# Kernel optimization log

Hardware: AMD Instinct MI355X
Metric: run time of the kernel (lower is better)

The kernel has to match this reference:

```python
import jax, jax.numpy as jnp
import numpy as np

N_PIXELS = 262144
N_CENTERS = 1024
N_G = 256

def setup_inputs() -> dict:
    key = jax.random.key(0)
    k1, k2, k3, k4, k5 = jax.random.split(key, 5)
    return {
        "alphas": jax.random.normal(k1, (N_CENTERS, 1), dtype=jnp.float32),
        "betas": jax.random.normal(k2, (N_G, 2), dtype=jnp.float32) * 0.1,
        "K": jax.random.normal(k3, (N_PIXELS, N_G), dtype=jnp.float32) * 0.05,
        "all_pixels": jax.random.normal(k4, (N_PIXELS, 2), dtype=jnp.float32),
        "all_p_centers": jax.random.normal(k5, (N_CENTERS, 2), dtype=jnp.float32),
        "sdp2": jnp.ones((), dtype=jnp.float32) * 2.0,
    }

def reference(alphas, betas, K, all_pixels, all_p_centers, sdp2):
    # deformed pixel coordinates: (n_pixels, 2)
    deformed = all_pixels - K @ betas
    # pairwise squared distances via norm expansion (same math as the torch
    # ones-matmul broadcasting, expressed with plain broadcasting):
    p_norm2 = jnp.sum(jnp.square(deformed), axis=1, keepdims=True)      # (n_pixels, 1)
    c_norm2 = jnp.sum(jnp.square(all_p_centers), axis=1)                # (n_centers,)
    p_dot_c = 2.0 * (deformed @ all_p_centers.T)                        # (n_pixels, n_centers)
    big_matrix = p_norm2 + c_norm2[None, :] - p_dot_c
    kBp = jnp.exp(-big_matrix / (2.0 * sdp2))
    return kBp @ alphas                                                  # (n_pixels, 1)
```

## Files before the change

kernel.cpp:

```cpp
#include <hip/hip_runtime.h>

#if defined(__has_builtin)
#  if __has_builtin(__builtin_amdgcn_exp2f)
#    define EXP2F(x) __builtin_amdgcn_exp2f(x)
#  else
#    define EXP2F(x) exp2f(x)
#  endif
#else
#  define EXP2F(x) exp2f(x)
#endif

constexpr int NPIX  = 262144;
constexpr int NC    = 1024;
constexpr int NG    = 256;
constexpr int BLOCK = 256;
constexpr int PIX_PER_BLOCK = 256;

template <int CTRL>
__device__ __forceinline__ float dpp_add(float v) {
    union { float f; int i; } u, t;
    u.f = v;
    t.i = __builtin_amdgcn_update_dpp(0, u.i, CTRL, 0xF, 0xF, true);
    return v + t.f;
}
template <int CTRL>
__device__ __forceinline__ float dpp_mov(float v) {
    union { float f; int i; } u, t;
    u.f = v;
    t.i = __builtin_amdgcn_update_dpp(0, u.i, CTRL, 0xF, 0xF, true);
    return t.f;
}
__device__ __forceinline__ float sum16(float v) {
    v = dpp_add<0xB1>(v);
    v = dpp_add<0x4E>(v);
    v = dpp_add<0x141>(v);
    v = dpp_add<0x140>(v);
    return v;
}

__global__ void prep_centers(const float* __restrict__ alphas,
                             const float* __restrict__ centers,
                             const float* __restrict__ sdp2p,
                             float* __restrict__ ws)
{
    const int c = blockIdx.x * blockDim.x + threadIdx.x;
    if (c < NC) {
        const float f  = -1.44269504088896340736f / (2.0f * sdp2p[0]);
        const float cx = centers[2 * c + 0];
        const float cy = centers[2 * c + 1];
        ws[c]          = cx;
        ws[NC + c]     = cy;
        ws[2 * NC + c] = alphas[c] * EXP2F(f * (cx * cx + cy * cy));
    }
}

__global__ __launch_bounds__(BLOCK, 4)
void kbpa_main(const float* __restrict__ betas,
               const float* __restrict__ K,
               const float* __restrict__ pixels,
               const float* __restrict__ sdp2p,
               const float* __restrict__ ws,
               float* __restrict__ out)
{
    const int tid  = threadIdx.x;
    const int lane = tid & 63;
    const int wave = tid >> 6;
    const int l4   = lane & 15;
    const int lg   = lane >> 4;
    const int own  = l4 * 4 + lg;

    const float f   = -1.44269504088896340736f / (2.0f * sdp2p[0]);
    const float m2f = -2.0f * f;

    const float4* wcx4 = (const float4*)(ws);
    const float4* wcy4 = (const float4*)(ws + NC);
    const float4* wca4 = (const float4*)(ws + 2 * NC);
    float4 rcx[4], rcy[4], rca[4];
    #pragma unroll
    for (int j = 0; j < 4; ++j) {
        rcx[j] = wcx4[lane * 4 + j];
        rcy[j] = wcy4[lane * 4 + j];
        rca[j] = wca4[lane * 4 + j];
    }

    const float4* bf4 = (const float4*)betas;
    float4 b0[4], b1[4];
    #pragma unroll
    for (int k = 0; k < 4; ++k) {
        b0[k] = bf4[l4 * 2 + k * 32];
        b1[k] = bf4[l4 * 2 + k * 32 + 1];
    }

    const int g0 = blockIdx.x * PIX_PER_BLOCK + wave * 64;
    const float2 mypix = ((const float2*)pixels)[g0 + own];

    float dx = 0.f, dy = 0.f;
    #pragma unroll 2
    for (int it = 0; it < 16; ++it) {
        const float4* kr = (const float4*)(K + (size_t)(g0 + it * 4 + lg) * NG);
        float4 kv[4];
        #pragma unroll
        for (int k = 0; k < 4; ++k) kv[k] = kr[l4 + 16 * k];
        float sx = 0.f, sy = 0.f;
        #pragma unroll
        for (int k = 0; k < 4; ++k) {
            sx = fmaf(kv[k].x, b0[k].x, sx); sy = fmaf(kv[k].x, b0[k].y, sy);
            sx = fmaf(kv[k].y, b0[k].z, sx); sy = fmaf(kv[k].y, b0[k].w, sy);
            sx = fmaf(kv[k].z, b1[k].x, sx); sy = fmaf(kv[k].z, b1[k].y, sy);
            sx = fmaf(kv[k].w, b1[k].z, sx); sy = fmaf(kv[k].w, b1[k].w, sy);
        }
        sx = sum16(sx); sy = sum16(sy);
        if (l4 == it) { dx = mypix.x - sx; dy = mypix.y - sy; }
    }

    float dxs = m2f * dx, dys = m2f * dy, acc = 0.f;
    #pragma unroll 1
    for (int round = 0; round < 4; ++round) {
        #pragma unroll 2
        for (int t = 0; t < 16; ++t) {
            float t0 = 0.f, t1 = 0.f, t2 = 0.f, t3 = 0.f;
            #pragma unroll
            for (int j = 0; j < 4; ++j) {
                t0 = fmaf(rca[j].x, EXP2F(fmaf(dxs, rcx[j].x, dys * rcy[j].x)), t0);
                t1 = fmaf(rca[j].y, EXP2F(fmaf(dxs, rcx[j].y, dys * rcy[j].y)), t1);
                t2 = fmaf(rca[j].z, EXP2F(fmaf(dxs, rcx[j].z, dys * rcy[j].z)), t2);
                t3 = fmaf(rca[j].w, EXP2F(fmaf(dxs, rcx[j].w, dys * rcy[j].w)), t3);
            }
            acc += (t0 + t1) + (t2 + t3);
            dxs = dpp_mov<0x121>(dxs);
            dys = dpp_mov<0x121>(dys);
            acc = dpp_mov<0x121>(acc);
        }
        const int sw = lane ^ ((round & 1) ? 32 : 16);
        dxs = __shfl(dxs, sw);
        dys = __shfl(dys, sw);
        acc = __shfl(acc, sw);
    }

    out[g0 + own] = acc * EXP2F(f * (dx * dx + dy * dy));
}

extern "C" void kernel_launch(void* const* d_in, const int* in_sizes, int n_in,
                              void* d_out, int out_size, void* d_ws, size_t ws_size,
                              hipStream_t stream)
{
    const float* alphas  = (const float*)d_in[0];
    const float* betas   = (const float*)d_in[1];
    const float* K       = (const float*)d_in[2];
    const float* pixels  = (const float*)d_in[3];
    const float* centers = (const float*)d_in[4];
    const float* sdp2    = (const float*)d_in[5];
    float* outp          = (float*)d_out;
    float* ws            = (float*)d_ws;

    hipLaunchKernelGGL(prep_centers, dim3(NC / 256), dim3(256), 0, stream,
                       alphas, centers, sdp2, ws);
    hipLaunchKernelGGL(kbpa_main, dim3(NPIX / PIX_PER_BLOCK), dim3(BLOCK), 0, stream,
                       betas, K, pixels, sdp2, ws, outp);
}
```

Measured before the change: 81.55 us.

## Split fused deform+RBF kernel into separate deformation and RBF kernels

Separates the K@betas deformation reduction from the exp-based RBF accumulation into two kernels, passing the deformation offsets through workspace memory. The deform kernel gives each wave 32 rows, launched over 2048 blocks, while the RBF kernel maps one pixel per lane with contiguous loads. The aim is to let each phase run with its own simpler, lower-register code and better access patterns. In exchange it loses the overlap of the memory-bound K stream with the exp-bound compute inside one kernel. It also adds a launch and a small intermediate write and read.

Measured after the change: 85.83 us. 1.05x slower.

```diff
diff --git a/kernel.cpp b/kernel.cpp
--- a/kernel.cpp
+++ b/kernel.cpp
@@ -13,8 +13,6 @@
 constexpr int NPIX  = 262144;
 constexpr int NC    = 1024;
 constexpr int NG    = 256;
-constexpr int BLOCK = 256;
-constexpr int PIX_PER_BLOCK = 256;
 
 template <int CTRL>
 __device__ __forceinline__ float dpp_add(float v) {
@@ -38,6 +36,8 @@
     return v;
 }
 
+constexpr int WS_SXY_OFF = 4096;
+
 __global__ void prep_centers(const float* __restrict__ alphas,
                              const float* __restrict__ centers,
                              const float* __restrict__ sdp2p,
@@ -54,20 +54,57 @@
     }
 }
 
-__global__ __launch_bounds__(BLOCK, 4)
-void kbpa_main(const float* __restrict__ betas,
-               const float* __restrict__ K,
-               const float* __restrict__ pixels,
-               const float* __restrict__ sdp2p,
-               const float* __restrict__ ws,
-               float* __restrict__ out)
+constexpr int BLOCKS_A = 2048;
+__global__ __launch_bounds__(256, 4)
+void deform_k(const float* __restrict__ betas,
+              const float* __restrict__ K,
+              float2* __restrict__ sxy)
 {
     const int tid  = threadIdx.x;
     const int lane = tid & 63;
     const int wave = tid >> 6;
     const int l4   = lane & 15;
     const int lg   = lane >> 4;
-    const int own  = l4 * 4 + lg;
+
+    const float4* bf4 = (const float4*)betas;
+    float4 b0[4], b1[4];
+    #pragma unroll
+    for (int k = 0; k < 4; ++k) {
+        b0[k] = bf4[l4 * 2 + k * 32];
+        b1[k] = bf4[l4 * 2 + k * 32 + 1];
+    }
+
+    const int base = (blockIdx.x * 4 + wave) * 32;
+
+    #pragma unroll 2
+    for (int it = 0; it < 8; ++it) {
+        const float4* kr = (const float4*)(K + (size_t)(base + it * 4 + lg) * NG);
+        float4 kv[4];
+        #pragma unroll
+        for (int k = 0; k < 4; ++k) kv[k] = kr[l4 + 16 * k];
+        float sx = 0.f, sy = 0.f;
+        #pragma unroll
+        for (int k = 0; k < 4; ++k) {
+            sx = fmaf(kv[k].x, b0[k].x, sx); sy = fmaf(kv[k].x, b0[k].y, sy);
+            sx = fmaf(kv[k].y, b0[k].z, sx); sy = fmaf(kv[k].y, b0[k].w, sy);
+            sx = fmaf(kv[k].z, b1[k].x, sx); sy = fmaf(kv[k].z, b1[k].y, sy);
+            sx = fmaf(kv[k].w, b1[k].z, sx); sy = fmaf(kv[k].w, b1[k].w, sy);
+        }
+        sx = sum16(sx); sy = sum16(sy);
+        if (l4 == it) sxy[base + it * 4 + lg] = make_float2(sx, sy);
+    }
+}
+
+__global__ __launch_bounds__(256, 4)
+void rbf_k(const float* __restrict__ pixels,
+           const float* __restrict__ sdp2p,
+           const float* __restrict__ ws,
+           float* __restrict__ out)
+{
+    const int tid  = threadIdx.x;
+    const int lane = tid & 63;
+    const int wave = tid >> 6;
+    const int p    = blockIdx.x * 256 + wave * 64 + lane;
 
     const float f   = -1.44269504088896340736f / (2.0f * sdp2p[0]);
     const float m2f = -2.0f * f;
@@ -83,35 +120,10 @@
         rca[j] = wca4[lane * 4 + j];
     }
 
-    const float4* bf4 = (const float4*)betas;
-    float4 b0[4], b1[4];
-    #pragma unroll
-    for (int k = 0; k < 4; ++k) {
-        b0[k] = bf4[l4 * 2 + k * 32];
-        b1[k] = bf4[l4 * 2 + k * 32 + 1];
-    }
-
-    const int g0 = blockIdx.x * PIX_PER_BLOCK + wave * 64;
-    const float2 mypix = ((const float2*)pixels)[g0 + own];
-
-    float dx = 0.f, dy = 0.f;
-    #pragma unroll 2
-    for (int it = 0; it < 16; ++it) {
-        const float4* kr = (const float4*)(K + (size_t)(g0 + it * 4 + lg) * NG);
-        float4 kv[4];
-        #pragma unroll
-        for (int k = 0; k < 4; ++k) kv[k] = kr[l4 + 16 * k];
-        float sx = 0.f, sy = 0.f;
-        #pragma unroll
-        for (int k = 0; k < 4; ++k) {
-            sx = fmaf(kv[k].x, b0[k].x, sx); sy = fmaf(kv[k].x, b0[k].y, sy);
-            sx = fmaf(kv[k].y, b0[k].z, sx); sy = fmaf(kv[k].y, b0[k].w, sy);
-            sx = fmaf(kv[k].z, b1[k].x, sx); sy = fmaf(kv[k].z, b1[k].y, sy);
-            sx = fmaf(kv[k].w, b1[k].z, sx); sy = fmaf(kv[k].w, b1[k].w, sy);
-        }
-        sx = sum16(sx); sy = sum16(sy);
-        if (l4 == it) { dx = mypix.x - sx; dy = mypix.y - sy; }
-    }
+    const float2 s  = ((const float2*)(ws + WS_SXY_OFF))[p];
+    const float2 px = ((const float2*)pixels)[p];
+    const float dx = px.x - s.x;
+    const float dy = px.y - s.y;
 
     float dxs = m2f * dx, dys = m2f * dy, acc = 0.f;
     #pragma unroll 1
@@ -137,7 +149,7 @@
         acc = __shfl(acc, sw);
     }
 
-    out[g0 + own] = acc * EXP2F(f * (dx * dx + dy * dy));
+    out[p] = acc * EXP2F(f * (dx * dx + dy * dy));
 }
 
 extern "C" void kernel_launch(void* const* d_in, const int* in_sizes, int n_in,
@@ -155,6 +167,8 @@
 
     hipLaunchKernelGGL(prep_centers, dim3(NC / 256), dim3(256), 0, stream,
                        alphas, centers, sdp2, ws);
-    hipLaunchKernelGGL(kbpa_main, dim3(NPIX / PIX_PER_BLOCK), dim3(BLOCK), 0, stream,
-                       betas, K, pixels, sdp2, ws, outp);
+    hipLaunchKernelGGL(deform_k, dim3(BLOCKS_A), dim3(256), 0, stream,
+                       betas, K, (float2*)(ws + WS_SXY_OFF));
+    hipLaunchKernelGGL(rbf_k, dim3(NPIX / 256), dim3(256), 0, stream,
+                       pixels, sdp2, ws, outp);
 }
```
